# Kernel tuning notes

Measured on AMD Instinct MI355X. Metric: run time of the kernel, lower is better.

## Reference

```python
import jax, jax.numpy as jnp
import numpy as np

B, T, N_EMBD, HEAD_SIZE = 4, 4096, 32, 32


def setup_inputs() -> dict:
    key = jax.random.key(0)
    k1, k2, k3, k4 = jax.random.split(key, 4)
    x = jax.random.normal(k1, (B, T, N_EMBD), dtype=jnp.float32)
    Wq = jax.random.normal(k2, (HEAD_SIZE, N_EMBD), dtype=jnp.float32) * (N_EMBD ** -0.5)
    Wk = jax.random.normal(k3, (HEAD_SIZE, N_EMBD), dtype=jnp.float32) * (N_EMBD ** -0.5)
    Wv = jax.random.normal(k4, (HEAD_SIZE, N_EMBD), dtype=jnp.float32) * (N_EMBD ** -0.5)
    return {"x": x, "Wq": Wq, "Wk": Wk, "Wv": Wv}


def reference(x, Wq, Wk, Wv):
    # Linear(bias=False): y = x @ W.T  -> [B, T, head_size]
    q = jnp.einsum('btn,hn->bth', x, Wq)
    k = jnp.einsum('btn,hn->bth', x, Wk)
    v = jnp.einsum('btn,hn->bth', x, Wv)
    scale = q.shape[-1] ** -0.5
    # [B, T, T] attention scores
    wei = jnp.einsum('bth,bsh->bts', q, k) * scale
    # Faithful to source: tril the scores, then mask entries equal to 0
    tril = jnp.tril(wei)
    wei = jax.nn.softmax(jnp.where(tril == 0, -jnp.inf, tril), axis=-1)
    return jnp.einsum('bts,bsh->bth', wei, v)
```

## Files before the change

kernel.cpp:

```cpp
#include <hip/hip_runtime.h>
#include <cmath>

#define BB 4
#define TT 4096
#define NE 32
#define HS 32

#define IPB 2176
#define MAXSP 16
#define SLOT 288
#define FNEG (-1.0e30f)

typedef unsigned int uint32;
typedef __fp16 half2v __attribute__((ext_vector_type(2)));
typedef __fp16 half4v __attribute__((ext_vector_type(4)));
typedef __fp16 half8v __attribute__((ext_vector_type(8)));
typedef float f32x4 __attribute__((ext_vector_type(4)));

__device__ __forceinline__ half2v u2h(uint32 u) {
    union { uint32 u; half2v h; } x; x.u = u; return x.h;
}

#if __has_builtin(__builtin_amdgcn_cvt_pkrtz)
__device__ __forceinline__ half2v pkf16(float a, float b) {
    return __builtin_amdgcn_cvt_pkrtz(a, b);
}
#else
__device__ __forceinline__ half2v pkf16(float a, float b) {
    half2v h; h.x = (__fp16)a; h.y = (__fp16)b; return h;
}
#endif

__global__ __launch_bounds__(256) void qkv_proj(
    const float* __restrict__ x,
    const float* __restrict__ Wq,
    const float* __restrict__ Wk,
    const float* __restrict__ Wv,
    __fp16* __restrict__ Qh, __fp16* __restrict__ Kh,
    __fp16* __restrict__ Vt4)
{
    int tid = blockIdx.x * 256 + threadIdx.x;
    int row = tid >> 5;
    int h   = tid & 31;
    const float4* xr4 = reinterpret_cast<const float4*>(x + (size_t)row * NE);
    float4 xv4[8];
    #pragma unroll
    for (int k = 0; k < 8; ++k) xv4[k] = xr4[k];
    const float* xv = (const float*)xv4;
    float aq = 0.f, ak = 0.f, av = 0.f;
    #pragma unroll
    for (int d = 0; d < NE; ++d) {
        aq = fmaf(xv[d], Wq[h * NE + d], aq);
        ak = fmaf(xv[d], Wk[h * NE + d], ak);
        av = fmaf(xv[d], Wv[h * NE + d], av);
    }
    size_t o = (size_t)row * HS + h;
    Qh[o] = (__fp16)aq;
    Kh[o] = (__fp16)ak;
    int b = row >> 12, t = row & (TT - 1);
    Vt4[((size_t)(b * (TT / 4) + (t >> 2)) * HS + h) * 4 + (t & 3)] = (__fp16)av;
}

__global__ __launch_bounds__(256) void attn_partial(
    const __fp16* __restrict__ Qh, const __fp16* __restrict__ Kh,
    const __fp16* __restrict__ Vt4, float* __restrict__ part)
{
    const float SC2 = 0.17677669529663687f * 1.4426950408889634f;

    int wave = threadIdx.x >> 6;
    int lane = threadIdx.x & 63;
    int item = blockIdx.x * 4 + wave;
    int b = item / IPB;
    int r = item - b * IPB;
    int g = (int)((sqrtf((float)(4 + 2 * r)) - 2.0f) * 0.25f);
    if (g < 0) g = 0;
    while (8 * (g + 1) * (g + 2) <= r) ++g;
    while (8 * g * (g + 1) > r) --g;
    int rr = r - 8 * g * (g + 1);
    int tq = rr / (g + 1);
    int t  = 16 * g + tq;
    int sp = rr - tq * (g + 1);
    int qt0 = t * 16;
    int kbase = sp * 256;
    int kend  = min(kbase + 256, qt0 + 16);
    int nsub  = (kend - kbase) >> 4;

    int c = lane & 15;
    int q = lane >> 4;

    const __fp16* Qb = Qh  + (size_t)b * TT * HS;
    const __fp16* Kb = Kh  + (size_t)b * TT * HS;
    const __fp16* Vb = Vt4 + (size_t)b * (TT / 4) * HS * 4;

    union U4H8 { uint4 u; half8v h; };
    union U2H4 { uint2 u; half4v h; };
    union H4   { half4v h4; half2v h2[2]; };
    union H2U2 { half2v h[2]; uint2 u; };

    U4H8 qf; qf.u = *(const uint4*)(Qb + (size_t)(qt0 + c) * HS + 8 * q);

    float m = FNEG, l = 0.0f;
    f32x4 oh0 = {0.f, 0.f, 0.f, 0.f};
    f32x4 oh1 = {0.f, 0.f, 0.f, 0.f};
    const f32x4 zero = {0.f, 0.f, 0.f, 0.f};

    auto do16 = [&](int kb) {
        U4H8 kf; kf.u = *(const uint4*)(Kb + (size_t)(kb + c) * HS + 8 * q);
        const __fp16* vrow = Vb + (size_t)((kb >> 2) + q) * (HS * 4);
        U2H4 vf0; vf0.u = *(const uint2*)(vrow + c * 4);
        U2H4 vf1; vf1.u = *(const uint2*)(vrow + (c + 16) * 4);
        f32x4 s = __builtin_amdgcn_mfma_f32_16x16x32_f16(kf.h, qf.h, zero, 0, 0, 0);
        bool diag = (kb == qt0);
        float w[4];
        #pragma unroll
        for (int j = 0; j < 4; ++j) {
            w[j] = (s[j] != 0.0f) ? s[j] * SC2 : FNEG;
            if (diag && (4 * q + j > c)) w[j] = FNEG;
        }
        float tmax = fmaxf(fmaxf(w[0], w[1]), fmaxf(w[2], w[3]));
        tmax = fmaxf(tmax, __shfl_xor(tmax, 16));
        tmax = fmaxf(tmax, __shfl_xor(tmax, 32));
        if (__any(tmax > m)) {
            float mn = fmaxf(m, tmax);
            float alpha = exp2f(m - mn);
            l *= alpha; oh0 *= alpha; oh1 *= alpha; m = mn;
        }
        float p0 = exp2f(w[0] - m), p1 = exp2f(w[1] - m);
        float p2 = exp2f(w[2] - m), p3 = exp2f(w[3] - m);
        l += (p0 + p1) + (p2 + p3);
        H4 pf; pf.h2[0] = pkf16(p0, p1); pf.h2[1] = pkf16(p2, p3);
        oh0 = __builtin_amdgcn_mfma_f32_16x16x16f16(vf0.h, pf.h4, oh0, 0, 0, 0);
        oh1 = __builtin_amdgcn_mfma_f32_16x16x16f16(vf1.h, pf.h4, oh1, 0, 0, 0);
    };

    auto do32 = [&](int kb) {
        U4H8 kfa; kfa.u = *(const uint4*)(Kb + (size_t)(kb + c) * HS + 8 * q);
        U4H8 kfb; kfb.u = *(const uint4*)(Kb + (size_t)(kb + 16 + c) * HS + 8 * q);
        const __fp16* vrowa = Vb + (size_t)((kb >> 2) + q) * (HS * 4);
        const __fp16* vrowb = vrowa + 4 * (HS * 4);
        U2H4 va0; va0.u = *(const uint2*)(vrowa + c * 4);
        U2H4 va1; va1.u = *(const uint2*)(vrowa + (c + 16) * 4);
        U2H4 vb0; vb0.u = *(const uint2*)(vrowb + c * 4);
        U2H4 vb1; vb1.u = *(const uint2*)(vrowb + (c + 16) * 4);
        f32x4 sa = __builtin_amdgcn_mfma_f32_16x16x32_f16(kfa.h, qf.h, zero, 0, 0, 0);
        f32x4 sb = __builtin_amdgcn_mfma_f32_16x16x32_f16(kfb.h, qf.h, zero, 0, 0, 0);
        bool diaga = (kb == qt0), diagb = (kb + 16 == qt0);
        float wa[4], wb[4];
        #pragma unroll
        for (int j = 0; j < 4; ++j) {
            wa[j] = (sa[j] != 0.0f) ? sa[j] * SC2 : FNEG;
            wb[j] = (sb[j] != 0.0f) ? sb[j] * SC2 : FNEG;
            if (diaga && (4 * q + j > c)) wa[j] = FNEG;
            if (diagb && (4 * q + j > c)) wb[j] = FNEG;
        }
        float ta = fmaxf(fmaxf(wa[0], wa[1]), fmaxf(wa[2], wa[3]));
        float tb = fmaxf(fmaxf(wb[0], wb[1]), fmaxf(wb[2], wb[3]));
        float tmax = fmaxf(ta, tb);
        tmax = fmaxf(tmax, __shfl_xor(tmax, 16));
        tmax = fmaxf(tmax, __shfl_xor(tmax, 32));
        if (__any(tmax > m)) {
            float mn = fmaxf(m, tmax);
            float alpha = exp2f(m - mn);
            l *= alpha; oh0 *= alpha; oh1 *= alpha; m = mn;
        }
        float pa0 = exp2f(wa[0] - m), pa1 = exp2f(wa[1] - m);
        float pa2 = exp2f(wa[2] - m), pa3 = exp2f(wa[3] - m);
        float pb0 = exp2f(wb[0] - m), pb1 = exp2f(wb[1] - m);
        float pb2 = exp2f(wb[2] - m), pb3 = exp2f(wb[3] - m);
        l += ((pa0 + pa1) + (pa2 + pa3)) + ((pb0 + pb1) + (pb2 + pb3));
        H4 pfa; pfa.h2[0] = pkf16(pa0, pa1); pfa.h2[1] = pkf16(pa2, pa3);
        H4 pfb; pfb.h2[0] = pkf16(pb0, pb1); pfb.h2[1] = pkf16(pb2, pb3);
        oh0 = __builtin_amdgcn_mfma_f32_16x16x16f16(va0.h, pfa.h4, oh0, 0, 0, 0);
        oh1 = __builtin_amdgcn_mfma_f32_16x16x16f16(va1.h, pfa.h4, oh1, 0, 0, 0);
        oh0 = __builtin_amdgcn_mfma_f32_16x16x16f16(vb0.h, pfb.h4, oh0, 0, 0, 0);
        oh1 = __builtin_amdgcn_mfma_f32_16x16x16f16(vb1.h, pfb.h4, oh1, 0, 0, 0);
    };

    if (nsub == 16) {
        #pragma unroll 2
        for (int pp = 0; pp < 8; ++pp) do32(kbase + 32 * pp);
    } else {
        int kb = kbase;
        int np = nsub >> 1;
        for (int pp = 0; pp < np; ++pp) { do32(kb); kb += 32; }
        if (nsub & 1) do16(kb);
    }

    float lt = l + __shfl_xor(l, 16);
    lt += __shfl_xor(lt, 32);

    float* P = part + (size_t)((b * 256 + t) * MAXSP + sp) * SLOT;
    if (q == 0) { P[c] = m; P[16 + c] = lt; }
    uint32* Od = (uint32*)(P + 32) + c * 16 + 2 * q;
    H2U2 a;
    a.h[0] = pkf16(oh0[0], oh0[1]); a.h[1] = pkf16(oh0[2], oh0[3]);
    *(uint2*)Od = a.u;
    a.h[0] = pkf16(oh1[0], oh1[1]); a.h[1] = pkf16(oh1[2], oh1[3]);
    *(uint2*)(Od + 8) = a.u;
}

__global__ __launch_bounds__(256) void attn_combine(
    const float* __restrict__ part, float* __restrict__ out)
{
    int tid = blockIdx.x * 256 + threadIdx.x;
    int hq = tid & 3;
    int c  = (tid >> 2) & 15;
    int t  = (tid >> 6) & 255;
    int b  = tid >> 14;
    int ns = (t >> 4) + 1;

    const float* base = part + (size_t)(b * 256 + t) * MAXSP * SLOT;

    float M = FNEG;
    for (int s = 0; s < ns; ++s) M = fmaxf(M, base[(size_t)s * SLOT + c]);

    float acc[8];
    #pragma unroll
    for (int k = 0; k < 8; ++k) acc[k] = 0.f;
    float L = 0.f;
    for (int s = 0; s < ns; ++s) {
        const float* P = base + (size_t)s * SLOT;
        float ms = P[c], ls = P[16 + c];
        float wgt = (ls > 0.0f) ? exp2f(ms - M) : 0.0f;
        L += ls * wgt;
        uint4 ov = *(const uint4*)((const uint32*)(P + 32) + c * 16 + 4 * hq);
        const uint32* ovp = (const uint32*)&ov;
        #pragma unroll
        for (int pr = 0; pr < 4; ++pr) {
            half2v hh = u2h(ovp[pr]);
            acc[2 * pr]     = fmaf((float)hh.x, wgt, acc[2 * pr]);
            acc[2 * pr + 1] = fmaf((float)hh.y, wgt, acc[2 * pr + 1]);
        }
    }
    float invL = 1.0f / L;
    float* orow = out + ((size_t)(b * TT + t * 16 + c)) * HS + 8 * hq;
    float4 o0 = {acc[0] * invL, acc[1] * invL, acc[2] * invL, acc[3] * invL};
    float4 o1 = {acc[4] * invL, acc[5] * invL, acc[6] * invL, acc[7] * invL};
    *(float4*)orow = o0;
    *(float4*)(orow + 4) = o1;
}

extern "C" void kernel_launch(void* const* d_in, const int* in_sizes, int n_in,
                              void* d_out, int out_size, void* d_ws, size_t ws_size,
                              hipStream_t stream)
{
    const float* x  = (const float*)d_in[0];
    const float* Wq = (const float*)d_in[1];
    const float* Wk = (const float*)d_in[2];
    const float* Wv = (const float*)d_in[3];
    float* out = (float*)d_out;

    __fp16* Qh  = (__fp16*)d_ws;
    __fp16* Kh  = Qh + (size_t)BB * TT * HS;
    __fp16* Vt4 = Kh + (size_t)BB * TT * HS;
    float* part = (float*)(Vt4 + (size_t)BB * TT * HS);

    qkv_proj<<<dim3((BB * TT * HS) / 256), dim3(256), 0, stream>>>(
        x, Wq, Wk, Wv, Qh, Kh, Vt4);
    attn_partial<<<dim3((BB * IPB) / 4), dim3(256), 0, stream>>>(
        Qh, Kh, Vt4, part);
    attn_combine<<<dim3(256), dim3(256), 0, stream>>>(part, out);
}
```

Before: 126.4 us.

## Split each wave's key range into two independent online-softmax streams

Each wave now processes its key span as two halves, each with its own running max, sum and output accumulators, and interleaves do32 calls between them. The two chains merge with rescaling before the partial result is written. The aim is more instruction-level parallelism, so one stream's MFMA, exp and reduction latency hides behind the other's. A launch bound of 5 waves-per-EU caps register use to hold occupancy, and the combine kernel drops its ls>0 guard, which could produce NaN or inf for fully masked rows.

Result: faster. 119.7 us (-5.3%).

```diff
diff --git a/kernel.cpp b/kernel.cpp
--- a/kernel.cpp
+++ b/kernel.cpp
@@ -61,7 +61,7 @@
     Vt4[((size_t)(b * (TT / 4) + (t >> 2)) * HS + h) * 4 + (t & 3)] = (__fp16)av;
 }
 
-__global__ __launch_bounds__(256) void attn_partial(
+__global__ __launch_bounds__(256, 5) void attn_partial(
     const __fp16* __restrict__ Qh, const __fp16* __restrict__ Kh,
     const __fp16* __restrict__ Vt4, float* __restrict__ part)
 {
@@ -99,12 +99,11 @@
 
     U4H8 qf; qf.u = *(const uint4*)(Qb + (size_t)(qt0 + c) * HS + 8 * q);
 
-    float m = FNEG, l = 0.0f;
-    f32x4 oh0 = {0.f, 0.f, 0.f, 0.f};
-    f32x4 oh1 = {0.f, 0.f, 0.f, 0.f};
     const f32x4 zero = {0.f, 0.f, 0.f, 0.f};
-
-    auto do16 = [&](int kb) {
+    float mA = FNEG, lA = 0.f, mB = FNEG, lB = 0.f;
+    f32x4 oA0 = zero, oA1 = zero, oB0 = zero, oB1 = zero;
+
+    auto do16 = [&](int kb, float& m, float& l, f32x4& o0, f32x4& o1) {
         U4H8 kf; kf.u = *(const uint4*)(Kb + (size_t)(kb + c) * HS + 8 * q);
         const __fp16* vrow = Vb + (size_t)((kb >> 2) + q) * (HS * 4);
         U2H4 vf0; vf0.u = *(const uint2*)(vrow + c * 4);
@@ -123,17 +122,17 @@
         if (__any(tmax > m)) {
             float mn = fmaxf(m, tmax);
             float alpha = exp2f(m - mn);
-            l *= alpha; oh0 *= alpha; oh1 *= alpha; m = mn;
+            l *= alpha; o0 *= alpha; o1 *= alpha; m = mn;
         }
         float p0 = exp2f(w[0] - m), p1 = exp2f(w[1] - m);
         float p2 = exp2f(w[2] - m), p3 = exp2f(w[3] - m);
         l += (p0 + p1) + (p2 + p3);
         H4 pf; pf.h2[0] = pkf16(p0, p1); pf.h2[1] = pkf16(p2, p3);
-        oh0 = __builtin_amdgcn_mfma_f32_16x16x16f16(vf0.h, pf.h4, oh0, 0, 0, 0);
-        oh1 = __builtin_amdgcn_mfma_f32_16x16x16f16(vf1.h, pf.h4, oh1, 0, 0, 0);
+        o0 = __builtin_amdgcn_mfma_f32_16x16x16f16(vf0.h, pf.h4, o0, 0, 0, 0);
+        o1 = __builtin_amdgcn_mfma_f32_16x16x16f16(vf1.h, pf.h4, o1, 0, 0, 0);
     };
 
-    auto do32 = [&](int kb) {
+    auto do32 = [&](int kb, float& m, float& l, f32x4& o0, f32x4& o1) {
         U4H8 kfa; kfa.u = *(const uint4*)(Kb + (size_t)(kb + c) * HS + 8 * q);
         U4H8 kfb; kfb.u = *(const uint4*)(Kb + (size_t)(kb + 16 + c) * HS + 8 * q);
         const __fp16* vrowa = Vb + (size_t)((kb >> 2) + q) * (HS * 4);
@@ -161,7 +160,7 @@
         if (__any(tmax > m)) {
             float mn = fmaxf(m, tmax);
             float alpha = exp2f(m - mn);
-            l *= alpha; oh0 *= alpha; oh1 *= alpha; m = mn;
+            l *= alpha; o0 *= alpha; o1 *= alpha; m = mn;
         }
         float pa0 = exp2f(wa[0] - m), pa1 = exp2f(wa[1] - m);
         float pa2 = exp2f(wa[2] - m), pa3 = exp2f(wa[3] - m);
@@ -170,32 +169,56 @@
         l += ((pa0 + pa1) + (pa2 + pa3)) + ((pb0 + pb1) + (pb2 + pb3));
         H4 pfa; pfa.h2[0] = pkf16(pa0, pa1); pfa.h2[1] = pkf16(pa2, pa3);
         H4 pfb; pfb.h2[0] = pkf16(pb0, pb1); pfb.h2[1] = pkf16(pb2, pb3);
-        oh0 = __builtin_amdgcn_mfma_f32_16x16x16f16(va0.h, pfa.h4, oh0, 0, 0, 0);
-        oh1 = __builtin_amdgcn_mfma_f32_16x16x16f16(va1.h, pfa.h4, oh1, 0, 0, 0);
-        oh0 = __builtin_amdgcn_mfma_f32_16x16x16f16(vb0.h, pfb.h4, oh0, 0, 0, 0);
-        oh1 = __builtin_amdgcn_mfma_f32_16x16x16f16(vb1.h, pfb.h4, oh1, 0, 0, 0);
+        o0 = __builtin_amdgcn_mfma_f32_16x16x16f16(va0.h, pfa.h4, o0, 0, 0, 0);
+        o1 = __builtin_amdgcn_mfma_f32_16x16x16f16(va1.h, pfa.h4, o1, 0, 0, 0);
+        o0 = __builtin_amdgcn_mfma_f32_16x16x16f16(vb0.h, pfb.h4, o0, 0, 0, 0);
+        o1 = __builtin_amdgcn_mfma_f32_16x16x16f16(vb1.h, pfb.h4, o1, 0, 0, 0);
     };
+
+    int nA = (nsub + 1) >> 1;
+    int nB = nsub - nA;
+    int aB = kbase, bB = kbase + 16 * nA;
 
     if (nsub == 16) {
         #pragma unroll 2
-        for (int pp = 0; pp < 8; ++pp) do32(kbase + 32 * pp);
+        for (int i = 0; i < 4; ++i) {
+            do32(aB + 32 * i, mA, lA, oA0, oA1);
+            do32(bB + 32 * i, mB, lB, oB0, oB1);
+        }
     } else {
-        int kb = kbase;
-        int np = nsub >> 1;
-        for (int pp = 0; pp < np; ++pp) { do32(kb); kb += 32; }
-        if (nsub & 1) do16(kb);
+        int na32 = nA >> 1, nb32 = nB >> 1;
+        int np = min(na32, nb32);
+        for (int i = 0; i < np; ++i) {
+            do32(aB + 32 * i, mA, lA, oA0, oA1);
+            do32(bB + 32 * i, mB, lB, oB0, oB1);
+        }
+        for (int i = np; i < na32; ++i) do32(aB + 32 * i, mA, lA, oA0, oA1);
+        for (int i = np; i < nb32; ++i) do32(bB + 32 * i, mB, lB, oB0, oB1);
+        if (nA & 1) do16(aB + 32 * na32, mA, lA, oA0, oA1);
+        if (nB & 1) do16(bB + 32 * nb32, mB, lB, oB0, oB1);
+    }
+
+    float mm = fmaxf(mA, mB);
+    float wgtA = exp2f(mA - mm);
+    float wgtB = exp2f(mB - mm);
+    float l = lA * wgtA + lB * wgtB;
+    f32x4 o0, o1;
+    #pragma unroll
+    for (int k = 0; k < 4; ++k) {
+        o0[k] = oA0[k] * wgtA + oB0[k] * wgtB;
+        o1[k] = oA1[k] * wgtA + oB1[k] * wgtB;
     }
 
     float lt = l + __shfl_xor(l, 16);
     lt += __shfl_xor(lt, 32);
 
     float* P = part + (size_t)((b * 256 + t) * MAXSP + sp) * SLOT;
-    if (q == 0) { P[c] = m; P[16 + c] = lt; }
+    if (q == 0) { P[c] = mm; P[16 + c] = lt; }
     uint32* Od = (uint32*)(P + 32) + c * 16 + 2 * q;
     H2U2 a;
-    a.h[0] = pkf16(oh0[0], oh0[1]); a.h[1] = pkf16(oh0[2], oh0[3]);
+    a.h[0] = pkf16(o0[0], o0[1]); a.h[1] = pkf16(o0[2], o0[3]);
     *(uint2*)Od = a.u;
-    a.h[0] = pkf16(oh1[0], oh1[1]); a.h[1] = pkf16(oh1[2], oh1[3]);
+    a.h[0] = pkf16(o1[0], o1[1]); a.h[1] = pkf16(o1[2], o1[3]);
     *(uint2*)(Od + 8) = a.u;
 }
 
@@ -221,7 +244,7 @@
     for (int s = 0; s < ns; ++s) {
         const float* P = base + (size_t)s * SLOT;
         float ms = P[c], ls = P[16 + c];
-        float wgt = (ls > 0.0f) ? exp2f(ms - M) : 0.0f;
+        float wgt = exp2f(ms - M);
         L += ls * wgt;
         uint4 ov = *(const uint4*)((const uint32*)(P + 32) + c * 16 + 4 * hq);
         const uint32* ovp = (const uint32*)&ov;
```
